# Optimization experiments

Hardware: AMD Instinct MI355X
Metric: run time of the kernel (lower is better)

## Reference

```python
import jax, jax.numpy as jnp
import numpy as np

B, S, H, F, V, MAX_OOV = 128, 512, 1024, 512, 50000, 50


def setup_inputs() -> dict:
    key = jax.random.key(0)
    ks = jax.random.split(key, 20)
    r = lambda i, shp, s=0.02: (jax.random.normal(ks[i], shp, jnp.float32) * s)
    return dict(
        input=jax.random.randint(ks[0], (B,), 0, V),
        hidden=jax.random.normal(ks[1], (1, B, H), jnp.float32) * 0.1,
        encoder_outputs=jax.random.normal(ks[2], (B, S, H), jnp.float32) * 0.1,
        x_padding_masks=jnp.ones((B, S), jnp.float32),
        len_oov=jax.random.randint(ks[3], (B,), 0, MAX_OOV),
        coverage_vector=jnp.zeros((B, S), jnp.float32),
        ref2tgt=jax.random.randint(ks[4], (B, S), 0, V + MAX_OOV),
        emb=r(5, (V, F)),
        W_ih=r(6, (3 * H, F)), W_hh=r(7, (3 * H, H)),
        b_ih=jnp.zeros(3 * H, jnp.float32), b_hh=jnp.zeros(3 * H, jnp.float32),
        e2v1_w=r(8, (F, H)), e2v1_b=jnp.zeros(F, jnp.float32),
        e2v2_w=r(9, (V, F)), e2v2_b=jnp.zeros(V, jnp.float32),
        fc_w=r(10, (H, 2 * H)), fc_b=jnp.zeros(H, jnp.float32),
        wgen_w=r(11, (1, 2 * H + F)), wgen_b=jnp.zeros(1, jnp.float32),
        att_Wh=r(12, (H, H)), att_Ws=r(13, (H, H)),
        att_wc=r(14, (H,)), att_b=jnp.zeros(H, jnp.float32), att_v=r(15, (H,)),
    )


def reference(input, hidden, encoder_outputs, x_padding_masks, len_oov,
              coverage_vector, ref2tgt, emb, W_ih, W_hh, b_ih, b_hh,
              e2v1_w, e2v1_b, e2v2_w, e2v2_b, fc_w, fc_b, wgen_w, wgen_b,
              att_Wh, att_Ws, att_wc, att_b, att_v):
    # embedding lookup (dropout is identity at inference)
    emb_x = emb[input]  # [B, F]

    # --- additive (Bahdanau) attention with coverage ---
    s = hidden[0]  # [B, H] (n_layers == 1)
    feat = jnp.tanh(
        jnp.einsum('bsh,kh->bsk', encoder_outputs, att_Wh)
        + (s @ att_Ws.T)[:, None, :]
        + coverage_vector[:, :, None] * att_wc
        + att_b)  # [B, S, H]
    e = jnp.einsum('bsh,h->bs', feat, att_v)  # [B, S]
    a = jax.nn.softmax(e, axis=1) * x_padding_masks
    a = a / (jnp.sum(a, axis=1, keepdims=True))  # [B, S] renormalized attn
    coverage_new = coverage_vector + a
    context = jnp.einsum('bs,bsh->bh', a, encoder_outputs)  # [B, H]
    h_att = jnp.concatenate([s, context], axis=-1) @ fc_w.T + fc_b  # [B, H]

    # --- single-step GRU (PyTorch gate order r, z, n) ---
    gi = emb_x @ W_ih.T + b_ih  # [B, 3H]
    gh = h_att @ W_hh.T + b_hh  # [B, 3H]
    i_r, i_z, i_n = jnp.split(gi, 3, axis=-1)
    h_r, h_z, h_n = jnp.split(gh, 3, axis=-1)
    r = jax.nn.sigmoid(i_r + h_r)
    z = jax.nn.sigmoid(i_z + h_z)
    n = jnp.tanh(i_n + r * h_n)
    h_new = (1.0 - z) * n + z * h_att  # [B, H]

    # --- vocab distribution ---
    out1 = h_new @ e2v1_w.T + e2v1_b  # [B, F]
    p_vocab = jax.nn.softmax(out1 @ e2v2_w.T + e2v2_b, axis=1)  # [B, V]

    # --- pointer-generator mixing ---
    x_gen = jnp.concatenate([context, h_new, emb_x], axis=-1)  # [B, 2H+F]
    p_gen = jax.nn.sigmoid(x_gen @ wgen_w.T + wgen_b)[:, 0]  # [B]
    p_gen = jnp.clip(p_gen, 0.001, 0.999)
    p_vocab_w = p_gen[:, None] * p_vocab  # [B, V]
    attn_w = (1.0 - p_gen)[:, None] * a  # [B, S]
    p_ext = jnp.concatenate([p_vocab_w, jnp.zeros((B, MAX_OOV), p_vocab_w.dtype)], axis=1)
    rows = jnp.arange(B)[:, None]
    final = p_ext.at[rows, ref2tgt].add(attn_w)  # scatter_add over extended vocab

    return final, h_new[None], coverage_new, a
```

## Files before the change

kernel.cpp:

```cpp
#include <hip/hip_runtime.h>
#include <math.h>

#define B_   128
#define S_   512
#define H_   1024
#define F_   512
#define V_   50000
#define OOV_ 50
#define EV_  (V_ + OOV_)

#define BM 128
#define BN 128
#define BK 64

typedef __attribute__((ext_vector_type(8))) __bf16 bf16x8;
typedef __attribute__((ext_vector_type(4))) __bf16 bf16x4;
typedef __attribute__((ext_vector_type(4))) float  f32x4;

__device__ __forceinline__ void gload_lds16(const void* g, void* lds) {
  __builtin_amdgcn_global_load_lds(
      (const __attribute__((address_space(1))) unsigned int*)g,
      (__attribute__((address_space(3))) unsigned int*)lds, 16, 0, 0);
}

__device__ __forceinline__ float fast_tanh(float x) {
  float v = fminf(fmaxf(x, -15.f), 15.f);
  float t = __expf(2.f * v);
  return 1.f - 2.f / (t + 1.f);
}

__global__ __launch_bounds__(256)
void cast_both_kernel(const float* __restrict__ enc, __bf16* __restrict__ enc_h,
                      const float* __restrict__ wh, __bf16* __restrict__ wh_h)
{
  const size_t n_enc = (size_t)B_ * S_ * H_;
  const size_t n_tot = n_enc + (size_t)H_ * H_;
  for (size_t i = ((size_t)blockIdx.x * 256 + threadIdx.x) * 8; i < n_tot;
       i += (size_t)gridDim.x * 256 * 8) {
    const float* in; __bf16* out; size_t j;
    if (i < n_enc) { in = enc; out = enc_h; j = i; }
    else           { in = wh;  out = wh_h;  j = i - n_enc; }
    float4 a = *(const float4*)(in + j);
    float4 b = *(const float4*)(in + j + 4);
    bf16x8 o;
    o[0] = (__bf16)a.x; o[1] = (__bf16)a.y; o[2] = (__bf16)a.z; o[3] = (__bf16)a.w;
    o[4] = (__bf16)b.x; o[5] = (__bf16)b.y; o[6] = (__bf16)b.z; o[7] = (__bf16)b.w;
    *(bf16x8*)(out + j) = o;
  }
}

__global__ __launch_bounds__(256)
void gemm_splitk(const float* __restrict__ A, const float* __restrict__ W,
                 float* __restrict__ partial, int N, int K, int KS)
{
  __shared__ float As[128 * 68];
  __shared__ float Ws[32 * 68];
  const int tid = threadIdx.x;
  const int n0 = blockIdx.x * 32;
  const int p  = blockIdx.y;
  const int tx = tid & 7, ty = tid >> 3;
  const int lr = tid >> 4, lc4 = (tid & 15) * 4;
  float acc[4][4] = {};
  const int kend = p * KS + KS;
  for (int k0 = p * KS; k0 < kend; k0 += 64) {
#pragma unroll
    for (int pp = 0; pp < 8; ++pp)
      *(float4*)(As + (pp * 16 + lr) * 68 + lc4) =
          *(const float4*)(A + (size_t)(pp * 16 + lr) * K + k0 + lc4);
#pragma unroll
    for (int pp = 0; pp < 2; ++pp)
      *(float4*)(Ws + (pp * 16 + lr) * 68 + lc4) =
          *(const float4*)(W + (size_t)(n0 + pp * 16 + lr) * K + k0 + lc4);
    __syncthreads();
#pragma unroll
    for (int kk = 0; kk < 16; ++kk) {
      float4 av[4], wv[4];
#pragma unroll
      for (int i = 0; i < 4; i++) av[i] = *(const float4*)(As + (ty * 4 + i) * 68 + kk * 4);
#pragma unroll
      for (int j = 0; j < 4; j++) wv[j] = *(const float4*)(Ws + (tx * 4 + j) * 68 + kk * 4);
#pragma unroll
      for (int i = 0; i < 4; i++)
#pragma unroll
        for (int j = 0; j < 4; j++) {
          acc[i][j] = fmaf(av[i].x, wv[j].x, acc[i][j]);
          acc[i][j] = fmaf(av[i].y, wv[j].y, acc[i][j]);
          acc[i][j] = fmaf(av[i].z, wv[j].z, acc[i][j]);
          acc[i][j] = fmaf(av[i].w, wv[j].w, acc[i][j]);
        }
    }
    __syncthreads();
  }
#pragma unroll
  for (int i = 0; i < 4; i++)
#pragma unroll
    for (int j = 0; j < 4; j++)
      partial[((size_t)p * 128 + ty * 4 + i) * N + n0 + tx * 4 + j] = acc[i][j];
}

__global__ __launch_bounds__(256)
void gemm_splitk_cat(const float* __restrict__ A1, const float* __restrict__ A2,
                     const float* __restrict__ W, float* __restrict__ partial,
                     int N, int K, int KS)
{
  __shared__ float As[128 * 68];
  __shared__ float Ws[32 * 68];
  const int tid = threadIdx.x;
  const int n0 = blockIdx.x * 32;
  const int p  = blockIdx.y;
  const int tx = tid & 7, ty = tid >> 3;
  const int lr = tid >> 4, lc4 = (tid & 15) * 4;
  const float* A = (p * KS < 1024) ? A1 : A2;
  const int kbase = (p * KS < 1024) ? 0 : 1024;
  float acc[4][4] = {};
  const int kend = p * KS + KS;
  for (int k0 = p * KS; k0 < kend; k0 += 64) {
#pragma unroll
    for (int pp = 0; pp < 8; ++pp)
      *(float4*)(As + (pp * 16 + lr) * 68 + lc4) =
          *(const float4*)(A + (size_t)(pp * 16 + lr) * 1024 + (k0 - kbase) + lc4);
#pragma unroll
    for (int pp = 0; pp < 2; ++pp)
      *(float4*)(Ws + (pp * 16 + lr) * 68 + lc4) =
          *(const float4*)(W + (size_t)(n0 + pp * 16 + lr) * K + k0 + lc4);
    __syncthreads();
#pragma unroll
    for (int kk = 0; kk < 16; ++kk) {
      float4 av[4], wv[4];
#pragma unroll
      for (int i = 0; i < 4; i++) av[i] = *(const float4*)(As + (ty * 4 + i) * 68 + kk * 4);
#pragma unroll
      for (int j = 0; j < 4; j++) wv[j] = *(const float4*)(Ws + (tx * 4 + j) * 68 + kk * 4);
#pragma unroll
      for (int i = 0; i < 4; i++)
#pragma unroll
        for (int j = 0; j < 4; j++) {
          acc[i][j] = fmaf(av[i].x, wv[j].x, acc[i][j]);
          acc[i][j] = fmaf(av[i].y, wv[j].y, acc[i][j]);
          acc[i][j] = fmaf(av[i].z, wv[j].z, acc[i][j]);
          acc[i][j] = fmaf(av[i].w, wv[j].w, acc[i][j]);
        }
    }
    __syncthreads();
  }
#pragma unroll
  for (int i = 0; i < 4; i++)
#pragma unroll
    for (int j = 0; j < 4; j++)
      partial[((size_t)p * 128 + ty * 4 + i) * N + n0 + tx * 4 + j] = acc[i][j];
}

__global__ __launch_bounds__(256)
void gemm_splitk_gather(const int* __restrict__ input, const float* __restrict__ emb,
                        const float* __restrict__ W, float* __restrict__ partial,
                        int N, int K, int KS)
{
  __shared__ float As[128 * 68];
  __shared__ float Ws[32 * 68];
  const int tid = threadIdx.x;
  const int n0 = blockIdx.x * 32;
  const int p  = blockIdx.y;
  const int tx = tid & 7, ty = tid >> 3;
  const int lr = tid >> 4, lc4 = (tid & 15) * 4;
  float acc[4][4] = {};
  const int kend = p * KS + KS;
  for (int k0 = p * KS; k0 < kend; k0 += 64) {
#pragma unroll
    for (int pp = 0; pp < 8; ++pp) {
      int row = input[pp * 16 + lr];
      *(float4*)(As + (pp * 16 + lr) * 68 + lc4) =
          *(const float4*)(emb + (size_t)row * K + k0 + lc4);
    }
#pragma unroll
    for (int pp = 0; pp < 2; ++pp)
      *(float4*)(Ws + (pp * 16 + lr) * 68 + lc4) =
          *(const float4*)(W + (size_t)(n0 + pp * 16 + lr) * K + k0 + lc4);
    __syncthreads();
#pragma unroll
    for (int kk = 0; kk < 16; ++kk) {
      float4 av[4], wv[4];
#pragma unroll
      for (int i = 0; i < 4; i++) av[i] = *(const float4*)(As + (ty * 4 + i) * 68 + kk * 4);
#pragma unroll
      for (int j = 0; j < 4; j++) wv[j] = *(const float4*)(Ws + (tx * 4 + j) * 68 + kk * 4);
#pragma unroll
      for (int i = 0; i < 4; i++)
#pragma unroll
        for (int j = 0; j < 4; j++) {
          acc[i][j] = fmaf(av[i].x, wv[j].x, acc[i][j]);
          acc[i][j] = fmaf(av[i].y, wv[j].y, acc[i][j]);
          acc[i][j] = fmaf(av[i].z, wv[j].z, acc[i][j]);
          acc[i][j] = fmaf(av[i].w, wv[j].w, acc[i][j]);
        }
    }
    __syncthreads();
  }
#pragma unroll
  for (int i = 0; i < 4; i++)
#pragma unroll
    for (int j = 0; j < 4; j++)
      partial[((size_t)p * 128 + ty * 4 + i) * N + n0 + tx * 4 + j] = acc[i][j];
}

__global__ __launch_bounds__(256)
void reduce_partial(const float* __restrict__ partial, const float* __restrict__ bias,
                    float* __restrict__ C, int N, int P)
{
  int idx = blockIdx.x * 256 + threadIdx.x;
  int n = idx % N;
  float s = bias ? bias[n] : 0.f;
  for (int p = 0; p < P; ++p) s += partial[(size_t)p * 128 * N + idx];
  C[idx] = s;
}

__global__ __launch_bounds__(256)
void reduce_partial_bf16(const float* __restrict__ partial, const float* __restrict__ bias,
                         __bf16* __restrict__ C, int N, int P)
{
  int idx = blockIdx.x * 256 + threadIdx.x;
  int n = idx % N;
  float s = bias ? bias[n] : 0.f;
  for (int p = 0; p < P; ++p) s += partial[(size_t)p * 128 * N + idx];
  C[idx] = (__bf16)s;
}

__global__ __launch_bounds__(256, 2)
void feat_mfma_kernel(const __bf16* __restrict__ enc, const __bf16* __restrict__ Wh,
                      const float* __restrict__ sws, const float* __restrict__ cov,
                      const float* __restrict__ wcv, const float* __restrict__ ab,
                      const float* __restrict__ av_, float* __restrict__ e_part)
{
  __shared__ __attribute__((aligned(16))) __bf16 As[2][BM * BK];
  __shared__ __attribute__((aligned(16))) __bf16 Bs[2][BN * BK];
  __shared__ float red[BM][2];
  const int tid  = threadIdx.x;
  const int lane = tid & 63, wid = tid >> 6;
  const int wr = wid >> 1, wcc = wid & 1;
  const int bid = blockIdx.x;
  const int swz = (bid & 7) * 512 + (bid >> 3);
  const int bs0 = (swz >> 3) * BM;
  const int n0  = (swz & 7) * BN;
  const int b   = bs0 >> 9;

  const int scb = ((tid & 7) * 16) ^ (((tid >> 3) & 7) << 4);
  const __bf16* aPtr[2];
  const __bf16* aP[4]; const __bf16* bP[4]; int ldsO[4];
#pragma unroll
  for (int p = 0; p < 4; ++p) {
    int r = p * 32 + (tid >> 3);
    ldsO[p] = p * 4096 + tid * 16;
    aP[p] = enc + (size_t)(bs0 + r) * H_ + (scb >> 1);
    bP[p] = Wh  + (size_t)(n0  + r) * H_ + (scb >> 1);
  }
  (void)aPtr;

  const int swf = (lane & 7) << 4;
  int aO[4][2], bO[4][2];
#pragma unroll
  for (int m = 0; m < 4; ++m) {
    int rowa = wr * 64 + m * 16 + (lane & 15);
    int rowb = wcc * 64 + m * 16 + (lane & 15);
#pragma unroll
    for (int kk = 0; kk < 2; ++kk) {
      int kb = kk * 64 + ((lane >> 4) << 4);
      aO[m][kk] = rowa * 128 + (kb ^ swf);
      bO[m][kk] = rowb * 128 + (kb ^ swf);
    }
  }

  f32x4 acc[4][4];
#pragma unroll
  for (int i = 0; i < 4; i++)
#pragma unroll
    for (int j = 0; j < 4; j++) acc[i][j] = (f32x4){0.f, 0.f, 0.f, 0.f};

#define STAGE(c, ofs)                                                          \
  {                                                                            \
    _Pragma("unroll")                                                          \
    for (int p = 0; p < 4; ++p) {                                              \
      gload_lds16(aP[p] + (ofs), (char*)As[c] + ldsO[p]);                      \
      gload_lds16(bP[p] + (ofs), (char*)Bs[c] + ldsO[p]);                      \
    }                                                                          \
  }

#define COMPUTE(c)                                                             \
  {                                                                            \
    bf16x8 bfv[4][2];                                                          \
    _Pragma("unroll")                                                          \
    for (int n = 0; n < 4; ++n)                                                \
      _Pragma("unroll")                                                        \
      for (int kk = 0; kk < 2; ++kk)                                           \
        bfv[n][kk] = *(const bf16x8*)((const char*)Bs[c] + bO[n][kk]);         \
    _Pragma("unroll")                                                          \
    for (int m = 0; m < 4; ++m) {                                              \
      bf16x8 a0 = *(const bf16x8*)((const char*)As[c] + aO[m][0]);             \
      bf16x8 a1 = *(const bf16x8*)((const char*)As[c] + aO[m][1]);             \
      _Pragma("unroll")                                                        \
      for (int n = 0; n < 4; ++n) {                                            \
        acc[m][n] = __builtin_amdgcn_mfma_f32_16x16x32_bf16(a0, bfv[n][0], acc[m][n], 0, 0, 0); \
        acc[m][n] = __builtin_amdgcn_mfma_f32_16x16x32_bf16(a1, bfv[n][1], acc[m][n], 0, 0, 0); \
      }                                                                        \
    }                                                                          \
  }

  STAGE(0, 0)
  __syncthreads();

  for (int t2 = 0; t2 < 8; ++t2) {
    STAGE(1, 64)
    COMPUTE(0)
    __syncthreads();
    if (t2 < 7) STAGE(0, 128)
    COMPUTE(1)
    __syncthreads();
#pragma unroll
    for (int p = 0; p < 4; ++p) { aP[p] += 128; bP[p] += 128; }
  }
#undef STAGE
#undef COMPUTE

  float rowsum[4][4];
#pragma unroll
  for (int m = 0; m < 4; m++)
#pragma unroll
    for (int j = 0; j < 4; j++) rowsum[m][j] = 0.f;

#pragma unroll
  for (int n = 0; n < 4; ++n) {
    int col_g = n0 + wcc * 64 + n * 16 + (lane & 15);
    float sw   = sws[(size_t)b * H_ + col_g];
    float wc_n = wcv[col_g], ab_n = ab[col_g], av_n = av_[col_g];
#pragma unroll
    for (int m = 0; m < 4; ++m) {
#pragma unroll
      for (int j = 0; j < 4; ++j) {
        int row_l = wr * 64 + m * 16 + ((lane >> 4) << 2) + j;
        float val = acc[m][n][j] + sw + cov[bs0 + row_l] * wc_n + ab_n;
        rowsum[m][j] += fast_tanh(val) * av_n;
      }
    }
  }
#pragma unroll
  for (int m = 0; m < 4; ++m)
#pragma unroll
    for (int j = 0; j < 4; ++j) {
      float v = rowsum[m][j];
      v += __shfl_xor(v, 1);
      v += __shfl_xor(v, 2);
      v += __shfl_xor(v, 4);
      v += __shfl_xor(v, 8);
      rowsum[m][j] = v;
    }
  if ((lane & 15) == 0) {
#pragma unroll
    for (int m = 0; m < 4; ++m)
#pragma unroll
      for (int j = 0; j < 4; ++j)
        red[wr * 64 + m * 16 + ((lane >> 4) << 2) + j][wcc] = rowsum[m][j];
  }
  __syncthreads();
  if (tid < BM)
    e_part[(size_t)(swz & 7) * (B_ * S_) + bs0 + tid] = red[tid][0] + red[tid][1];
}

__global__ __launch_bounds__(256)
void logits_mfma_kernel(const __bf16* __restrict__ A, const float* __restrict__ W,
                        const float* __restrict__ bias, float* __restrict__ out0)
{
  __shared__ __attribute__((aligned(16))) __bf16 As[BM * BK];
  __shared__ __attribute__((aligned(16))) __bf16 Bs[BN * BK];
  const int tid  = threadIdx.x;
  const int lane = tid & 63, wid = tid >> 6;
  const int wr = wid >> 1, wcc = wid & 1;
  const int n0 = blockIdx.x * BN;

  f32x4 acc[4][4];
#pragma unroll
  for (int i = 0; i < 4; i++)
#pragma unroll
    for (int j = 0; j < 4; j++) acc[i][j] = (f32x4){0.f, 0.f, 0.f, 0.f};

  for (int k0 = 0; k0 < F_; k0 += BK) {
#pragma unroll
    for (int p = 0; p < 4; ++p) {
      int off = p * 4096 + tid * 16;
      int r = off >> 7, cb = off & 127;
      int scb = cb ^ ((r & 7) << 4);
      gload_lds16(A + (size_t)r * F_ + k0 + (scb >> 1), (char*)As + off);
    }
#pragma unroll
    for (int p = 0; p < 8; ++p) {
      int idx = p * 1024 + tid * 4;
      int r = idx >> 6, c = idx & 63;
      int row_g = n0 + r; if (row_g >= V_) row_g = V_ - 1;
      float4 f = *(const float4*)(W + (size_t)row_g * F_ + k0 + c);
      union { __bf16 h[4]; uint2 u; } t;
      t.h[0] = (__bf16)f.x; t.h[1] = (__bf16)f.y; t.h[2] = (__bf16)f.z; t.h[3] = (__bf16)f.w;
      int cb = c * 2;
      *(uint2*)((char*)Bs + r * 128 + (cb ^ ((r & 7) << 4))) = t.u;
    }
    __syncthreads();

    bf16x8 af[4][2], bfv[4][2];
#pragma unroll
    for (int m = 0; m < 4; ++m) {
      int row = wr * 64 + m * 16 + (lane & 15);
      int swz = (row & 7) << 4;
#pragma unroll
      for (int kk = 0; kk < 2; ++kk) {
        int kb = kk * 64 + ((lane >> 4) << 4);
        af[m][kk] = *(const bf16x8*)((const char*)As + row * 128 + (kb ^ swz));
      }
    }
#pragma unroll
    for (int n = 0; n < 4; ++n) {
      int row = wcc * 64 + n * 16 + (lane & 15);
      int swz = (row & 7) << 4;
#pragma unroll
      for (int kk = 0; kk < 2; ++kk) {
        int kb = kk * 64 + ((lane >> 4) << 4);
        bfv[n][kk] = *(const bf16x8*)((const char*)Bs + row * 128 + (kb ^ swz));
      }
    }
#pragma unroll
    for (int m = 0; m < 4; ++m)
#pragma unroll
      for (int n = 0; n < 4; ++n)
#pragma unroll
        for (int kk = 0; kk < 2; ++kk)
          acc[m][n] = __builtin_amdgcn_mfma_f32_16x16x32_bf16(af[m][kk], bfv[n][kk], acc[m][n], 0, 0, 0);
    __syncthreads();
  }

#pragma unroll
  for (int m = 0; m < 4; ++m) {
#pragma unroll
    for (int n = 0; n < 4; ++n) {
      int col_g = n0 + wcc * 64 + n * 16 + (lane & 15);
      if (col_g >= V_) continue;
      float bv = bias[col_g];
#pragma unroll
      for (int j = 0; j < 4; ++j) {
        int row = wr * 64 + m * 16 + ((lane >> 4) << 2) + j;
        out0[(size_t)row * EV_ + col_g] = acc[m][n][j] + bv;
      }
    }
  }
}

__global__ __launch_bounds__(512)
void softmax_a_kernel(const float* __restrict__ e_part, const float* __restrict__ mask,
                      const float* __restrict__ cov, float* __restrict__ a_ws,
                      float* __restrict__ out_a, float* __restrict__ out_cov)
{
  const int b = blockIdx.x;
  const int s = threadIdx.x;
  __shared__ float red[512];
  float e = 0.f;
  for (int kt = 0; kt < 8; ++kt) e += e_part[(size_t)kt * (B_ * S_) + b * S_ + s];
  red[s] = e;
  __syncthreads();
  for (int st = 256; st > 0; st >>= 1) {
    if (s < st) red[s] = fmaxf(red[s], red[s + st]);
    __syncthreads();
  }
  float mx = red[0];
  __syncthreads();
  float ex = expf(e - mx) * mask[b * S_ + s];
  red[s] = ex;
  __syncthreads();
  for (int st = 256; st > 0; st >>= 1) {
    if (s < st) red[s] += red[s + st];
    __syncthreads();
  }
  float a = ex / red[0];
  a_ws[b * S_ + s] = a;
  out_a[b * S_ + s] = a;
  out_cov[b * S_ + s] = cov[b * S_ + s] + a;
}

__global__ __launch_bounds__(256)
void context_kernel(const float* __restrict__ a_ws, const __bf16* __restrict__ enc,
                    float* __restrict__ ctx)
{
  const int b = blockIdx.y, q = blockIdx.x;
  const int lane = threadIdx.x & 63, w = threadIdx.x >> 6;
  const int h0 = q * 256 + lane * 4;
  __shared__ float al[S_];
  __shared__ float part[4][256];
  for (int i = threadIdx.x; i < S_; i += 256) al[i] = a_ws[b * S_ + i];
  __syncthreads();
  float acc0 = 0.f, acc1 = 0.f, acc2 = 0.f, acc3 = 0.f;
  const __bf16* ep = enc + (size_t)b * S_ * H_ + h0;
#pragma unroll 4
  for (int s = w * 128; s < w * 128 + 128; ++s) {
    bf16x4 v = *(const bf16x4*)(ep + (size_t)s * H_);
    float a = al[s];
    acc0 = fmaf(a, (float)v[0], acc0);
    acc1 = fmaf(a, (float)v[1], acc1);
    acc2 = fmaf(a, (float)v[2], acc2);
    acc3 = fmaf(a, (float)v[3], acc3);
  }
  part[w][lane * 4 + 0] = acc0;
  part[w][lane * 4 + 1] = acc1;
  part[w][lane * 4 + 2] = acc2;
  part[w][lane * 4 + 3] = acc3;
  __syncthreads();
  if (threadIdx.x < 256) {
    int o = threadIdx.x;
    ctx[b * H_ + q * 256 + o] = part[0][o] + part[1][o] + part[2][o] + part[3][o];
  }
}

__global__ __launch_bounds__(256)
void gru_kernel(const float* __restrict__ pgi, const float* __restrict__ pgh,
                const float* __restrict__ b_ih, const float* __restrict__ b_hh,
                const float* __restrict__ h_att, float* __restrict__ h_new_ws,
                float* __restrict__ out_h)
{
  int idx = blockIdx.x * 256 + threadIdx.x;
  int b = idx >> 10, h = idx & 1023;
  float ir = b_ih[h], iz = b_ih[H_ + h], in_ = b_ih[2 * H_ + h];
  float hr = b_hh[h], hz = b_hh[H_ + h], hn = b_hh[2 * H_ + h];
#pragma unroll
  for (int p = 0; p < 8; ++p) {
    const float* gp = pgi + (size_t)p * 128 * 3072 + (size_t)b * 3072;
    ir += gp[h]; iz += gp[H_ + h]; in_ += gp[2 * H_ + h];
    const float* hp = pgh + (size_t)p * 128 * 3072 + (size_t)b * 3072;
    hr += hp[h]; hz += hp[H_ + h]; hn += hp[2 * H_ + h];
  }
  float r = 1.f / (1.f + expf(-(ir + hr)));
  float z = 1.f / (1.f + expf(-(iz + hz)));
  float n = tanhf(in_ + r * hn);
  float ha = h_att[(size_t)b * H_ + h];
  float hv = (1.f - z) * n + z * ha;
  h_new_ws[idx] = hv;
  out_h[idx] = hv;
}

__global__ __launch_bounds__(512)
void stats_pgen_kernel(const float* __restrict__ logits, float* __restrict__ vmax,
                       float* __restrict__ vsum, const float* __restrict__ context,
                       const float* __restrict__ h_new, const int* __restrict__ input,
                       const float* __restrict__ emb, const float* __restrict__ wgen_w,
                       const float* __restrict__ wgen_b, float* __restrict__ pgen)
{
  __shared__ float red[512];
  if (blockIdx.x < B_) {
    int b = blockIdx.x;
    const float* row = logits + (size_t)b * EV_;
    float m = -1e30f;
    for (int v = threadIdx.x; v < V_; v += 512) m = fmaxf(m, row[v]);
    red[threadIdx.x] = m;
    __syncthreads();
    for (int st = 256; st > 0; st >>= 1) {
      if (threadIdx.x < st) red[threadIdx.x] = fmaxf(red[threadIdx.x], red[threadIdx.x + st]);
      __syncthreads();
    }
    m = red[0];
    __syncthreads();
    float ssum = 0.f;
    for (int v = threadIdx.x; v < V_; v += 512) ssum += expf(row[v] - m);
    red[threadIdx.x] = ssum;
    __syncthreads();
    for (int st = 256; st > 0; st >>= 1) {
      if (threadIdx.x < st) red[threadIdx.x] += red[threadIdx.x + st];
      __syncthreads();
    }
    if (threadIdx.x == 0) { vmax[b] = m; vsum[b] = red[0]; }
  } else {
    int b = blockIdx.x - B_;
    const float* erow = emb + (size_t)input[b] * F_;
    float acc = 0.f;
    for (int j = threadIdx.x; j < H_; j += 512) acc = fmaf(context[b * H_ + j], wgen_w[j], acc);
    for (int j = threadIdx.x; j < H_; j += 512) acc = fmaf(h_new[b * H_ + j], wgen_w[H_ + j], acc);
    for (int j = threadIdx.x; j < F_; j += 512) acc = fmaf(erow[j], wgen_w[2 * H_ + j], acc);
    red[threadIdx.x] = acc;
    __syncthreads();
    for (int st = 256; st > 0; st >>= 1) {
      if (threadIdx.x < st) red[threadIdx.x] += red[threadIdx.x + st];
      __syncthreads();
    }
    if (threadIdx.x == 0) {
      float p = 1.f / (1.f + expf(-(red[0] + wgen_b[0])));
      p = fminf(fmaxf(p, 0.001f), 0.999f);
      pgen[b] = p;
    }
  }
}

__global__ void final_kernel(float* __restrict__ out0, const float* __restrict__ vmax,
                             const float* __restrict__ vsum, const float* __restrict__ pgen)
{
  int b = blockIdx.y;
  int v = blockIdx.x * 256 + threadIdx.x;
  if (v >= EV_) return;
  float* row = out0 + (size_t)b * EV_;
  if (v < V_) row[v] = pgen[b] * expf(row[v] - vmax[b]) / vsum[b];
  else row[v] = 0.f;
}

__global__ void scatter_kernel(const int* __restrict__ ref2tgt, const float* __restrict__ a_ws,
                               const float* __restrict__ pgen, float* __restrict__ out0)
{
  int b = blockIdx.x;
  int s = threadIdx.x;
  float w = (1.f - pgen[b]) * a_ws[b * S_ + s];
  int t = ref2tgt[b * S_ + s];
  atomicAdd(&out0[(size_t)b * EV_ + t], w);
}

extern "C" void kernel_launch(void* const* d_in, const int* in_sizes, int n_in,
                              void* d_out, int out_size, void* d_ws, size_t ws_size,
                              hipStream_t stream)
{
  const int*   input   = (const int*)d_in[0];
  const float* hidden  = (const float*)d_in[1];
  const float* enc     = (const float*)d_in[2];
  const float* mask    = (const float*)d_in[3];
  const float* cov     = (const float*)d_in[5];
  const int*   ref2tgt = (const int*)d_in[6];
  const float* emb     = (const float*)d_in[7];
  const float* W_ih    = (const float*)d_in[8];
  const float* W_hh    = (const float*)d_in[9];
  const float* b_ih    = (const float*)d_in[10];
  const float* b_hh    = (const float*)d_in[11];
  const float* e2v1_w  = (const float*)d_in[12];
  const float* e2v1_b  = (const float*)d_in[13];
  const float* e2v2_w  = (const float*)d_in[14];
  const float* e2v2_b  = (const float*)d_in[15];
  const float* fc_w    = (const float*)d_in[16];
  const float* fc_b    = (const float*)d_in[17];
  const float* wgen_w  = (const float*)d_in[18];
  const float* wgen_b  = (const float*)d_in[19];
  const float* att_Wh  = (const float*)d_in[20];
  const float* att_Ws  = (const float*)d_in[21];
  const float* att_wc  = (const float*)d_in[22];
  const float* att_b   = (const float*)d_in[23];
  const float* att_v   = (const float*)d_in[24];

  char* w = (char*)d_ws;
  __bf16* enc_h  = (__bf16*)w;  w += (size_t)B_ * S_ * H_ * 2;
  __bf16* Wh_h   = (__bf16*)w;  w += (size_t)H_ * H_ * 2;
  __bf16* out1_h = (__bf16*)w;  w += (size_t)B_ * F_ * 2;
  float* sws     = (float*)w;   w += (size_t)B_ * H_ * 4;
  float* e_part  = (float*)w;   w += (size_t)8 * B_ * S_ * 4;
  float* a_ws    = (float*)w;   w += (size_t)B_ * S_ * 4;
  float* context = (float*)w;   w += (size_t)B_ * H_ * 4;
  float* h_att   = (float*)w;   w += (size_t)B_ * H_ * 4;
  float* h_new   = (float*)w;   w += (size_t)B_ * H_ * 4;
  float* pgen    = (float*)w;   w += 128 * 4;
  float* vmax    = (float*)w;   w += 128 * 4;
  float* vsum    = (float*)w;   w += 128 * 4;
  float* pA      = (float*)w;   w += (size_t)16 * 128 * 1024 * 4;
  float* pB      = (float*)w;   w += (size_t)8 * 128 * 3072 * 4;
  float* pC      = (float*)w;   w += (size_t)8 * 128 * 3072 * 4;

  float* out0    = (float*)d_out;
  float* out_h   = out0 + (size_t)B_ * EV_;
  float* out_cov = out_h + (size_t)B_ * H_;
  float* out_a   = out_cov + (size_t)B_ * S_;

  cast_both_kernel<<<4096, 256, 0, stream>>>(enc, enc_h, att_Wh, Wh_h);
  gemm_splitk<<<dim3(32, 16), 256, 0, stream>>>(hidden, att_Ws, pA, H_, H_, 64);
  reduce_partial<<<512, 256, 0, stream>>>(pA, nullptr, sws, H_, 16);
  feat_mfma_kernel<<<dim3(4096), 256, 0, stream>>>(enc_h, Wh_h, sws, cov, att_wc, att_b, att_v, e_part);
  softmax_a_kernel<<<B_, 512, 0, stream>>>(e_part, mask, cov, a_ws, out_a, out_cov);
  context_kernel<<<dim3(4, B_), 256, 0, stream>>>(a_ws, enc_h, context);
  gemm_splitk_cat<<<dim3(32, 16), 256, 0, stream>>>(hidden, context, fc_w, pA, H_, 2 * H_, 128);
  reduce_partial<<<512, 256, 0, stream>>>(pA, fc_b, h_att, H_, 16);
  gemm_splitk_gather<<<dim3(96, 8), 256, 0, stream>>>(input, emb, W_ih, pB, 3 * H_, F_, 64);
  gemm_splitk<<<dim3(96, 8), 256, 0, stream>>>(h_att, W_hh, pC, 3 * H_, H_, 128);
  gru_kernel<<<(B_ * H_) / 256, 256, 0, stream>>>(pB, pC, b_ih, b_hh, h_att, h_new, out_h);
  gemm_splitk<<<dim3(16, 16), 256, 0, stream>>>(h_new, e2v1_w, pA, F_, H_, 64);
  reduce_partial_bf16<<<256, 256, 0, stream>>>(pA, e2v1_b, out1_h, F_, 16);
  logits_mfma_kernel<<<dim3((V_ + BN - 1) / BN), 256, 0, stream>>>(out1_h, e2v2_w, e2v2_b, out0);
  stats_pgen_kernel<<<2 * B_, 512, 0, stream>>>(out0, vmax, vsum, context, h_new, input, emb,
                                                wgen_w, wgen_b, pgen);
  final_kernel<<<dim3((EV_ + 255) / 256, B_), 256, 0, stream>>>(out0, vmax, vsum, pgen);
  scatter_kernel<<<B_, 512, 0, stream>>>(ref2tgt, a_ws, pgen, out0);
}
```

Measured before the change: 511.7 us.

## Enlarge attention feature GEMM tile to 256x256 with deeper async pipelining

```diff
diff --git a/kernel.cpp b/kernel.cpp
--- a/kernel.cpp
+++ b/kernel.cpp
@@ -12,6 +12,10 @@
 #define BM 128
 #define BN 128
 #define BK 64
+
+#define BM2 256
+#define BN2 256
+#define BK2 64
 
 typedef __attribute__((ext_vector_type(8))) __bf16 bf16x8;
 typedef __attribute__((ext_vector_type(4))) __bf16 bf16x4;
@@ -224,53 +228,57 @@
   C[idx] = (__bf16)s;
 }
 
-__global__ __launch_bounds__(256, 2)
-void feat_mfma_kernel(const __bf16* __restrict__ enc, const __bf16* __restrict__ Wh,
-                      const float* __restrict__ sws, const float* __restrict__ cov,
-                      const float* __restrict__ wcv, const float* __restrict__ ab,
-                      const float* __restrict__ av_, float* __restrict__ e_part)
-{
-  __shared__ __attribute__((aligned(16))) __bf16 As[2][BM * BK];
-  __shared__ __attribute__((aligned(16))) __bf16 Bs[2][BN * BK];
-  __shared__ float red[BM][2];
+__global__ __launch_bounds__(512, 1)
+void feat_mfma256_kernel(const __bf16* __restrict__ enc, const __bf16* __restrict__ Wh,
+                         const float* __restrict__ sws, const float* __restrict__ cov,
+                         const float* __restrict__ wcv, const float* __restrict__ ab,
+                         const float* __restrict__ av_, float* __restrict__ e_part)
+{
+  __shared__ __attribute__((aligned(16))) __bf16 As[2][BM2 * BK2];
+  __shared__ __attribute__((aligned(16))) __bf16 Bs[2][BN2 * BK2];
   const int tid  = threadIdx.x;
   const int lane = tid & 63, wid = tid >> 6;
-  const int wr = wid >> 1, wcc = wid & 1;
+  const int wr = wid >> 2, wc = wid & 3;
   const int bid = blockIdx.x;
-  const int swz = (bid & 7) * 512 + (bid >> 3);
-  const int bs0 = (swz >> 3) * BM;
-  const int n0  = (swz & 7) * BN;
+  const int swz = (bid & 7) * 128 + (bid >> 3);
+  const int mt = swz >> 2, nt = swz & 3;
+  const int bs0 = mt * BM2;
+  const int n0  = nt * BN2;
   const int b   = bs0 >> 9;
 
   const int scb = ((tid & 7) * 16) ^ (((tid >> 3) & 7) << 4);
-  const __bf16* aPtr[2];
   const __bf16* aP[4]; const __bf16* bP[4]; int ldsO[4];
 #pragma unroll
   for (int p = 0; p < 4; ++p) {
-    int r = p * 32 + (tid >> 3);
-    ldsO[p] = p * 4096 + tid * 16;
+    int r = p * 64 + (tid >> 3);
+    ldsO[p] = p * 8192 + tid * 16;
     aP[p] = enc + (size_t)(bs0 + r) * H_ + (scb >> 1);
     bP[p] = Wh  + (size_t)(n0  + r) * H_ + (scb >> 1);
   }
-  (void)aPtr;
-
-  const int swf = (lane & 7) << 4;
-  int aO[4][2], bO[4][2];
-#pragma unroll
-  for (int m = 0; m < 4; ++m) {
-    int rowa = wr * 64 + m * 16 + (lane & 15);
-    int rowb = wcc * 64 + m * 16 + (lane & 15);
-#pragma unroll
-    for (int kk = 0; kk < 2; ++kk) {
-      int kb = kk * 64 + ((lane >> 4) << 4);
-      aO[m][kk] = rowa * 128 + (kb ^ swf);
-      bO[m][kk] = rowb * 128 + (kb ^ swf);
-    }
-  }
-
-  f32x4 acc[4][4];
-#pragma unroll
-  for (int i = 0; i < 4; i++)
+
+  const int lrow = lane & 15;
+  const int kbase = (lane >> 4) << 4;
+  int aO[8][2], bO[4][2];
+#pragma unroll
+  for (int m = 0; m < 8; ++m) {
+    int row = wr * 128 + m * 16 + lrow;
+    int sw = (row & 7) << 4;
+#pragma unroll
+    for (int kk = 0; kk < 2; ++kk)
+      aO[m][kk] = row * 128 + ((kk * 64 + kbase) ^ sw);
+  }
+#pragma unroll
+  for (int n = 0; n < 4; ++n) {
+    int row = wc * 64 + n * 16 + lrow;
+    int sw = (row & 7) << 4;
+#pragma unroll
+    for (int kk = 0; kk < 2; ++kk)
+      bO[n][kk] = row * 128 + ((kk * 64 + kbase) ^ sw);
+  }
+
+  f32x4 acc[8][4];
+#pragma unroll
+  for (int i = 0; i < 8; i++)
 #pragma unroll
     for (int j = 0; j < 4; j++) acc[i][j] = (f32x4){0.f, 0.f, 0.f, 0.f};
 
@@ -291,8 +299,9 @@
       _Pragma("unroll")                                                        \
       for (int kk = 0; kk < 2; ++kk)                                           \
         bfv[n][kk] = *(const bf16x8*)((const char*)Bs[c] + bO[n][kk]);         \
+    __builtin_amdgcn_s_setprio(1);                                             \
     _Pragma("unroll")                                                          \
-    for (int m = 0; m < 4; ++m) {                                              \
+    for (int m = 0; m < 8; ++m) {                                              \
       bf16x8 a0 = *(const bf16x8*)((const char*)As[c] + aO[m][0]);             \
       bf16x8 a1 = *(const bf16x8*)((const char*)As[c] + aO[m][1]);             \
       _Pragma("unroll")                                                        \
@@ -301,47 +310,69 @@
         acc[m][n] = __builtin_amdgcn_mfma_f32_16x16x32_bf16(a1, bfv[n][1], acc[m][n], 0, 0, 0); \
       }                                                                        \
     }                                                                          \
+    __builtin_amdgcn_s_setprio(0);                                             \
+  }
+
+#define VMCNT8() asm volatile("s_waitcnt vmcnt(8)" ::: "memory")
+#define VMCNT0() asm volatile("s_waitcnt vmcnt(0)" ::: "memory")
+#define BARRIER()                                                              \
+  {                                                                            \
+    __builtin_amdgcn_sched_barrier(0);                                         \
+    __builtin_amdgcn_s_barrier();                                              \
+    __builtin_amdgcn_sched_barrier(0);                                         \
   }
 
   STAGE(0, 0)
+  STAGE(1, 64)
+
+#pragma unroll 1
+  for (int t2 = 0; t2 < 7; ++t2) {
+    VMCNT8(); BARRIER();
+    COMPUTE(0)
+    BARRIER();
+    STAGE(0, 128)
+    VMCNT8(); BARRIER();
+    COMPUTE(1)
+    BARRIER();
+    STAGE(1, 192)
+#pragma unroll
+    for (int p = 0; p < 4; ++p) { aP[p] += 128; bP[p] += 128; }
+  }
+  VMCNT8(); BARRIER();
+  COMPUTE(0)
+  BARRIER();
+  VMCNT0(); BARRIER();
+  COMPUTE(1)
   __syncthreads();
-
-  for (int t2 = 0; t2 < 8; ++t2) {
-    STAGE(1, 64)
-    COMPUTE(0)
-    __syncthreads();
-    if (t2 < 7) STAGE(0, 128)
-    COMPUTE(1)
-    __syncthreads();
-#pragma unroll
-    for (int p = 0; p < 4; ++p) { aP[p] += 128; bP[p] += 128; }
-  }
 #undef STAGE
 #undef COMPUTE
-
-  float rowsum[4][4];
-#pragma unroll
-  for (int m = 0; m < 4; m++)
+#undef VMCNT8
+#undef VMCNT0
+#undef BARRIER
+
+  float rowsum[8][4];
+#pragma unroll
+  for (int m = 0; m < 8; m++)
 #pragma unroll
     for (int j = 0; j < 4; j++) rowsum[m][j] = 0.f;
 
 #pragma unroll
   for (int n = 0; n < 4; ++n) {
-    int col_g = n0 + wcc * 64 + n * 16 + (lane & 15);
+    int col_g = n0 + wc * 64 + n * 16 + (lane & 15);
     float sw   = sws[(size_t)b * H_ + col_g];
     float wc_n = wcv[col_g], ab_n = ab[col_g], av_n = av_[col_g];
 #pragma unroll
-    for (int m = 0; m < 4; ++m) {
+    for (int m = 0; m < 8; ++m) {
 #pragma unroll
       for (int j = 0; j < 4; ++j) {
-        int row_l = wr * 64 + m * 16 + ((lane >> 4) << 2) + j;
+        int row_l = wr * 128 + m * 16 + ((lane >> 4) << 2) + j;
         float val = acc[m][n][j] + sw + cov[bs0 + row_l] * wc_n + ab_n;
         rowsum[m][j] += fast_tanh(val) * av_n;
       }
     }
   }
 #pragma unroll
-  for (int m = 0; m < 4; ++m)
+  for (int m = 0; m < 8; ++m)
 #pragma unroll
     for (int j = 0; j < 4; ++j) {
       float v = rowsum[m][j];
@@ -351,16 +382,18 @@
       v += __shfl_xor(v, 8);
       rowsum[m][j] = v;
     }
+  float (*red)[4] = (float(*)[4])As;
   if ((lane & 15) == 0) {
 #pragma unroll
-    for (int m = 0; m < 4; ++m)
+    for (int m = 0; m < 8; ++m)
 #pragma unroll
       for (int j = 0; j < 4; ++j)
-        red[wr * 64 + m * 16 + ((lane >> 4) << 2) + j][wcc] = rowsum[m][j];
+        red[wr * 128 + m * 16 + ((lane >> 4) << 2) + j][wc] = rowsum[m][j];
   }
   __syncthreads();
-  if (tid < BM)
-    e_part[(size_t)(swz & 7) * (B_ * S_) + bs0 + tid] = red[tid][0] + red[tid][1];
+  if (tid < BM2)
+    e_part[(size_t)nt * (B_ * S_) + bs0 + tid] =
+        red[tid][0] + red[tid][1] + red[tid][2] + red[tid][3];
 }
 
 __global__ __launch_bounds__(256)
@@ -457,7 +490,7 @@
   const int s = threadIdx.x;
   __shared__ float red[512];
   float e = 0.f;
-  for (int kt = 0; kt < 8; ++kt) e += e_part[(size_t)kt * (B_ * S_) + b * S_ + s];
+  for (int kt = 0; kt < 4; ++kt) e += e_part[(size_t)kt * (B_ * S_) + b * S_ + s];
   red[s] = e;
   __syncthreads();
   for (int st = 256; st > 0; st >>= 1) {
@@ -664,7 +697,7 @@
   cast_both_kernel<<<4096, 256, 0, stream>>>(enc, enc_h, att_Wh, Wh_h);
   gemm_splitk<<<dim3(32, 16), 256, 0, stream>>>(hidden, att_Ws, pA, H_, H_, 64);
   reduce_partial<<<512, 256, 0, stream>>>(pA, nullptr, sws, H_, 16);
-  feat_mfma_kernel<<<dim3(4096), 256, 0, stream>>>(enc_h, Wh_h, sws, cov, att_wc, att_b, att_v, e_part);
+  feat_mfma256_kernel<<<dim3(1024), 512, 0, stream>>>(enc_h, Wh_h, sws, cov, att_wc, att_b, att_v, e_part);
   softmax_a_kernel<<<B_, 512, 0, stream>>>(e_part, mask, cov, a_ws, out_a, out_cov);
   context_kernel<<<dim3(4, B_), 256, 0, stream>>>(a_ws, enc_h, context);
   gemm_splitk_cat<<<dim3(32, 16), 256, 0, stream>>>(hidden, context, fc_w, pA, H_, 2 * H_, 128);
```

Measured after the change: 484.0 us. -5.4%, faster.
